# Kernel optimization log

Hardware: AMD Instinct MI355X
Metric: run time of the kernel (lower is better)

The kernel has to match this reference:

```python
import jax, jax.numpy as jnp
import numpy as np

X_DIM, Z_DIM, N_HEIGHT = 256, 256, 32
EPS = 1e-5  # BatchNorm1d eps

def _bn(x, g, b):
    # BatchNorm1d in training mode: batch statistics over the point axis
    m = x.mean(0)
    v = x.var(0)
    return (x - m) * jax.lax.rsqrt(v + EPS) * g + b

def setup_inputs() -> dict:
    key = jax.random.key(0)
    ks = jax.random.split(key, 16)
    B, N, F = 2, 120000, 3
    inp = {
        'pt_fea': jax.random.normal(ks[0], (B, N, F), jnp.float32),
        'grid_ind': jax.random.randint(ks[1], (B, N, 2), 0, 256, dtype=jnp.int32).astype(jnp.int64),
        'occupancy': (jax.random.uniform(ks[2], (B, 1, X_DIM, N_HEIGHT, Z_DIM)) < 0.1).astype(jnp.float32),
    }
    dims = [(3, 64), (64, 128), (128, 256), (256, 512)]
    for i, (di, do) in enumerate(dims):
        inp[f'W{i+1}'] = jax.random.normal(ks[3 + i], (di, do), jnp.float32) * 0.02
        inp[f'b{i+1}'] = jnp.zeros((do,), jnp.float32)
    for i, d in enumerate([3, 64, 128, 256]):
        inp[f'g{i}'] = jnp.ones((d,), jnp.float32)
        inp[f'be{i}'] = jnp.zeros((d,), jnp.float32)
    inp['Wc'] = jax.random.normal(ks[10], (512, 32), jnp.float32) * 0.02
    inp['bc'] = jnp.zeros((32,), jnp.float32)
    return inp

def reference(pt_fea, occupancy, W1, b1, W2, b2, W3, b3, W4, b4,
              g0, be0, g1, be1, g2, be2, g3, be3, Wc, bc, grid_ind):
    B, N, F = pt_fea.shape
    feats = pt_fea.reshape(B * N, F)                          # cat over batch
    # PointNet per-point MLP: BN -> (Linear -> BN -> ReLU) x3 -> Linear
    h = _bn(feats, g0, be0)
    h = jax.nn.relu(_bn(h @ W1 + b1, g1, be1))
    h = jax.nn.relu(_bn(h @ W2 + b2, g2, be2))
    h = jax.nn.relu(_bn(h @ W3 + b3, g3, be3))
    h = h @ W4 + b4                                           # [B*N, 512]

    # linear segment id per (batch, x, z) cell; equivalent to unique+scatter_max
    gi = grid_ind.reshape(B * N, 2).astype(jnp.int32)
    batch_idx = jnp.repeat(jnp.arange(B, dtype=jnp.int32), N)
    seg = batch_idx * (X_DIM * Z_DIM) + gi[:, 0] * Z_DIM + gi[:, 1]
    n_cells = B * X_DIM * Z_DIM

    pooled = jax.ops.segment_max(h, seg, num_segments=n_cells)          # [cells, 512]
    cnt = jax.ops.segment_sum(jnp.ones((B * N,), h.dtype), seg, num_segments=n_cells)
    occ_mask = (cnt > 0)[:, None]
    pooled = jnp.where(occ_mask, pooled, 0.0)                           # kill -inf empties

    # feature compression on occupied cells only; empty cells stay exactly 0
    comp = jax.nn.relu(pooled @ Wc + bc)
    comp = jnp.where(occ_mask, comp, 0.0)                               # [cells, 32]

    bev = comp.reshape(B, X_DIM, Z_DIM, -1).transpose(0, 3, 1, 2)       # [B, 32, X, Z]
    # MaxPool2d(k=3, stride=1, pad=1); -inf padding matches torch's implicit -inf pad
    bev = jax.lax.reduce_window(bev, -jnp.inf, jax.lax.max,
                                (1, 1, 3, 3), (1, 1, 1, 1), 'SAME')

    occu = occupancy[:, 0].transpose(0, 2, 1, 3)                        # [B, H, X, Z]
    out = jnp.concatenate([occu, bev], axis=1)                          # [B, H+32, X, Z]
    return out
```

## Files before the change

kernel.cpp:

```cpp
#include <hip/hip_runtime.h>
#include <hip/hip_bf16.h>

#define EPSN 1e-5f

typedef __bf16 bf16x8 __attribute__((ext_vector_type(8)));
typedef float f32x4 __attribute__((ext_vector_type(4)));

__device__ __forceinline__ unsigned encf(float f) {
  unsigned u = __float_as_uint(f);
  return (u & 0x80000000u) ? ~u : (u | 0x80000000u);
}
__device__ __forceinline__ float decf(unsigned u) {
  return (u & 0x80000000u) ? __uint_as_float(u ^ 0x80000000u) : __uint_as_float(~u);
}

__global__ __launch_bounds__(256) void stats_feats(const float* __restrict__ pt, int n,
                                                   float* __restrict__ sums) {
  float a0 = 0, a1 = 0, a2 = 0, q0 = 0, q1 = 0, q2 = 0;
  for (int p = blockIdx.x * 256 + threadIdx.x; p < n; p += gridDim.x * 256) {
    float v0 = pt[3 * p], v1 = pt[3 * p + 1], v2 = pt[3 * p + 2];
    a0 += v0; a1 += v1; a2 += v2;
    q0 += v0 * v0; q1 += v1 * v1; q2 += v2 * v2;
  }
  __shared__ float red[4][6];
  float vals[6] = {a0, a1, a2, q0, q1, q2};
  int lane = threadIdx.x & 63, wv = threadIdx.x >> 6;
#pragma unroll
  for (int k = 0; k < 6; k++) {
    float v = vals[k];
#pragma unroll
    for (int o = 32; o; o >>= 1) v += __shfl_down(v, o, 64);
    if (lane == 0) red[wv][k] = v;
  }
  __syncthreads();
  if (threadIdx.x < 6) {
    float v = red[0][threadIdx.x] + red[1][threadIdx.x] + red[2][threadIdx.x] + red[3][threadIdx.x];
    atomicAdd(&sums[threadIdx.x], v);
  }
}

__global__ void bn_prep(const float* __restrict__ sums, int C, float invN,
                        const float* __restrict__ g, const float* __restrict__ be,
                        float* __restrict__ sc, float* __restrict__ sh) {
  int c = threadIdx.x;
  if (c < C) {
    float m = sums[c] * invN;
    float v = fmaxf(sums[C + c] * invN - m * m, 0.f);
    float s = g[c] * rsqrtf(v + EPSN);
    sc[c] = s;
    sh[c] = be[c] - m * s;
  }
}

__global__ __launch_bounds__(256) void wconv(const float* __restrict__ W,
                                             __hip_bfloat16* __restrict__ Wt, int K, int C) {
  int idx = blockIdx.x * 256 + threadIdx.x;
  if (idx >= K * C) return;
  int k = idx / C, c = idx - k * C;
  Wt[(size_t)c * K + k] = __float2bfloat16(W[idx]);
}

__global__ __launch_bounds__(256) void gemm1_stats(const float* __restrict__ pt,
                                                   const float* __restrict__ W,
                                                   const float* __restrict__ bias,
                                                   const float* __restrict__ scsh,
                                                   __hip_bfloat16* __restrict__ Y,
                                                   int n, float* __restrict__ sums) {
  const int c = threadIdx.x & 63;
  const float w0 = W[c], w1 = W[64 + c], w2 = W[128 + c], bb = bias[c];
  const float s0 = scsh[0], s1 = scsh[1], s2 = scsh[2];
  const float h0 = scsh[4], h1 = scsh[5], h2 = scsh[6];
  float s = 0.f, q = 0.f;
  const int total = n * 64;
  for (int idx = blockIdx.x * 256 + threadIdx.x; idx < total; idx += gridDim.x * 256) {
    int p = idx >> 6;
    float x0 = s0 * pt[3 * p]     + h0;
    float x1 = s1 * pt[3 * p + 1] + h1;
    float x2 = s2 * pt[3 * p + 2] + h2;
    float y = bb + x0 * w0 + x1 * w1 + x2 * w2;
    Y[idx] = __float2bfloat16(y);
    s += y; q += y * y;
  }
  __shared__ float sred[4][64], qred[4][64];
  int wv = threadIdx.x >> 6;
  sred[wv][c] = s; qred[wv][c] = q;
  __syncthreads();
  if (threadIdx.x < 64) {
    float S = sred[0][c] + sred[1][c] + sred[2][c] + sred[3][c];
    float Q = qred[0][c] + qred[1][c] + qred[2][c] + qred[3][c];
    atomicAdd(&sums[c], S);
    atomicAdd(&sums[64 + c], Q);
  }
}

template <int K>
__global__ __launch_bounds__(256) void gemm_mfma(
    const __hip_bfloat16* __restrict__ Yin, const __hip_bfloat16* __restrict__ Wt,
    const float* __restrict__ bias, const float* __restrict__ sc, const float* __restrict__ sh,
    __hip_bfloat16* __restrict__ Yout, int C, float* __restrict__ sums, int nrows) {
  constexpr int KS = 64, LDA = 72, LDO = 80;
  __shared__ __align__(16) __hip_bfloat16 hA[128 * LDO];
  __shared__ float sredArr[128], qredArr[128];
  const int t = threadIdx.x;
  const int lane = t & 63, wv = t >> 6;
  const int mh = (wv >> 1) * 64, nh = (wv & 1) * 64;
  const int lm = lane & 15, lq = lane >> 4;
  const int p0 = blockIdx.x * 128;
  const int cb0 = blockIdx.y * 128;

  f32x4 acc[4][4];
#pragma unroll
  for (int i = 0; i < 4; i++)
#pragma unroll
    for (int j = 0; j < 4; j++) acc[i][j] = {0.f, 0.f, 0.f, 0.f};

  for (int k0 = 0; k0 < K; k0 += KS) {
    __syncthreads();
#pragma unroll
    for (int it = 0; it < 4; it++) {
      int idx = it * 256 + t;
      int row = idx >> 3;
      int c8 = (idx & 7) * 8;
      int gp = p0 + row;
      __hip_bfloat16 h8[8];
      if (gp < nrows) {
        uint4 raw = *(const uint4*)(Yin + (size_t)gp * K + k0 + c8);
        const __hip_bfloat16* pr = (const __hip_bfloat16*)&raw;
#pragma unroll
        for (int j = 0; j < 8; j++) {
          float v = sc[k0 + c8 + j] * __bfloat162float(pr[j]) + sh[k0 + c8 + j];
          h8[j] = __float2bfloat16(fmaxf(v, 0.f));
        }
      } else {
#pragma unroll
        for (int j = 0; j < 8; j++) h8[j] = __float2bfloat16(0.f);
      }
      *(uint4*)&hA[row * LDA + c8] = *(const uint4*)h8;
    }
    __syncthreads();
#pragma unroll
    for (int kk = 0; kk < KS; kk += 32) {
      bf16x8 a[4], b[4];
#pragma unroll
      for (int i = 0; i < 4; i++)
        a[i] = *(const bf16x8*)&hA[(mh + i * 16 + lm) * LDA + kk + lq * 8];
#pragma unroll
      for (int j = 0; j < 4; j++)
        b[j] = *(const bf16x8*)(const void*)(Wt + (size_t)(cb0 + nh + j * 16 + lm) * K + k0 + kk + lq * 8);
#pragma unroll
      for (int i = 0; i < 4; i++)
#pragma unroll
        for (int j = 0; j < 4; j++)
          acc[i][j] = __builtin_amdgcn_mfma_f32_16x16x32_bf16(a[i], b[j], acc[i][j], 0, 0, 0);
    }
  }

#pragma unroll
  for (int j = 0; j < 4; j++) {
    float bb = bias[cb0 + nh + j * 16 + lm];
#pragma unroll
    for (int i = 0; i < 4; i++)
#pragma unroll
      for (int r = 0; r < 4; r++) acc[i][j][r] += bb;
  }

  __syncthreads();
  if (t < 128) { sredArr[t] = 0.f; qredArr[t] = 0.f; }
  __syncthreads();

#pragma unroll
  for (int j = 0; j < 4; j++) {
    float s = 0.f, q = 0.f;
#pragma unroll
    for (int i = 0; i < 4; i++)
#pragma unroll
      for (int r = 0; r < 4; r++) {
        int grow = p0 + mh + i * 16 + lq * 4 + r;
        if (grow < nrows) { float v = acc[i][j][r]; s += v; q += v * v; }
      }
    s += __shfl_xor(s, 16); s += __shfl_xor(s, 32);
    q += __shfl_xor(q, 16); q += __shfl_xor(q, 32);
    if (lq == 0) {
      atomicAdd(&sredArr[nh + j * 16 + lm], s);
      atomicAdd(&qredArr[nh + j * 16 + lm], q);
    }
  }

  for (int half = 0; half < 2; half++) {
    __syncthreads();
    if ((wv & 1) == half) {
#pragma unroll
      for (int j = 0; j < 4; j++)
#pragma unroll
        for (int i = 0; i < 4; i++)
#pragma unroll
          for (int r = 0; r < 4; r++)
            hA[(mh + i * 16 + lq * 4 + r) * LDO + j * 16 + lm] = __float2bfloat16(acc[i][j][r]);
    }
    __syncthreads();
    int row = t >> 1, seg = t & 1;
    if (p0 + row < nrows) {
      const uint4* src = (const uint4*)&hA[row * LDO + seg * 32];
      uint4* dst = (uint4*)(Yout + (size_t)(p0 + row) * C + cb0 + half * 64 + seg * 32);
      dst[0] = src[0]; dst[1] = src[1]; dst[2] = src[2]; dst[3] = src[3];
    }
  }

  if (t < 128) {
    atomicAdd(&sums[cb0 + t], sredArr[t]);
    atomicAdd(&sums[C + cb0 + t], qredArr[t]);
  }
}

__global__ __launch_bounds__(256) void hist_kernel(const int* __restrict__ gi, int perB,
                                                   unsigned* __restrict__ hist) {
  int b = blockIdx.y;
  int p = blockIdx.x * 256 + threadIdx.x;
  if (p < perB) {
    int gp = b * perB + p;
    int c = (gi[2 * gp] & 255) * 256 + (gi[2 * gp + 1] & 255);
    atomicAdd(&hist[b * 65536 + c], 1u);
  }
}
__global__ __launch_bounds__(256) void scan1(const unsigned* __restrict__ hist,
                                             unsigned* __restrict__ cursor,
                                             unsigned* __restrict__ bSums) {
  __shared__ unsigned s[256];
  int b = blockIdx.y;
  int t = threadIdx.x, i = b * 65536 + blockIdx.x * 256 + t;
  unsigned v = hist[i]; s[t] = v; __syncthreads();
  for (int off = 1; off < 256; off <<= 1) {
    unsigned x = (t >= off) ? s[t - off] : 0u; __syncthreads();
    s[t] += x; __syncthreads();
  }
  cursor[i] = s[t] - v;
  if (t == 255) bSums[b * 256 + blockIdx.x] = s[255];
}
__global__ void scan2(unsigned* __restrict__ bSums) {
  __shared__ unsigned s[256];
  int t = threadIdx.x, i = blockIdx.x * 256 + t;
  unsigned v = bSums[i]; s[t] = v; __syncthreads();
  for (int off = 1; off < 256; off <<= 1) {
    unsigned x = (t >= off) ? s[t - off] : 0u; __syncthreads();
    s[t] += x; __syncthreads();
  }
  bSums[i] = s[t] - v;
}
__global__ __launch_bounds__(256) void mk_starts(const unsigned* __restrict__ cursor,
                                                 const unsigned* __restrict__ bSums,
                                                 unsigned* __restrict__ starts, int perB) {
  int b = blockIdx.y;
  int i = blockIdx.x * 256 + threadIdx.x;
  starts[b * 65537 + i] = cursor[b * 65536 + i] + bSums[b * 256 + (i >> 8)];
  if (i == 0) starts[b * 65537 + 65536] = (unsigned)perB;
}
__global__ __launch_bounds__(256) void scatter_kernel(const int* __restrict__ gi, int perB,
                                                      unsigned* __restrict__ cursor,
                                                      const unsigned* __restrict__ bSums,
                                                      unsigned* __restrict__ sorted,
                                                      unsigned* __restrict__ cells) {
  int b = blockIdx.y;
  int p = blockIdx.x * 256 + threadIdx.x;
  if (p < perB) {
    int gp = b * perB + p;
    int c = (gi[2 * gp] & 255) * 256 + (gi[2 * gp + 1] & 255);
    unsigned pos = atomicAdd(&cursor[b * 65536 + c], 1u) + bSums[b * 256 + (c >> 8)];
    if (pos < (unsigned)perB) {
      sorted[b * perB + pos] = (unsigned)p;
      cells[b * perB + pos] = (unsigned)c;
    }
  }
}

__global__ __launch_bounds__(256, 2) void pool_compress(
    const __hip_bfloat16* __restrict__ Y3, const __hip_bfloat16* __restrict__ Wt4,
    const float* __restrict__ b4, const float* __restrict__ sc, const float* __restrict__ sh,
    const __hip_bfloat16* __restrict__ WcT, const float* __restrict__ bc,
    const unsigned* __restrict__ sortedIdx, const unsigned* __restrict__ sortedCell,
    const unsigned* __restrict__ startsAll, float* __restrict__ comp, int perB) {
  constexpr int K = 256, KS = 64, LDA = 72, MLW = 516;
  __shared__ __align__(16) __hip_bfloat16 hA[64 * LDA];
  __shared__ __align__(16) unsigned maxLds[32 * MLW];
  __shared__ unsigned char slotRow[256];
  __shared__ int rowIdxLds[256];
  const int t = threadIdx.x;
  const int lane = t & 63, wv = t >> 6;
  const int lm = lane & 15, lq = lane >> 4;
  const int batch = blockIdx.y;
  const unsigned* starts = startsAll + batch * 65537;
  const int c0 = blockIdx.x * 32;
  const int r0 = (int)starts[c0];
  int n = (int)starts[c0 + 32] - r0;
  if (n > 256) n = 256;
  if (n < 0) n = 0;
  const int nrg = (n + 63) >> 6;

  for (int i = t; i < n; i += 256) {
    rowIdxLds[i] = (int)sortedIdx[batch * perB + r0 + i] + batch * perB;
    slotRow[i] = (unsigned char)((sortedCell[batch * perB + r0 + i] - c0) & 31);
  }
  for (int i = t; i < 32 * MLW; i += 256) maxLds[i] = 0u;

  for (int rg = 0; rg < nrg; rg++) {
    const int rbase = rg * 64;
    f32x4 acc[4][8];
#pragma unroll
    for (int i = 0; i < 4; i++)
#pragma unroll
      for (int j = 0; j < 8; j++) acc[i][j] = {0.f, 0.f, 0.f, 0.f};
    for (int k0 = 0; k0 < K; k0 += KS) {
      __syncthreads();
#pragma unroll
      for (int it = 0; it < 2; it++) {
        int idx = it * 256 + t;
        int row = idx >> 3;
        int c8 = (idx & 7) * 8;
        int gr = rbase + row;
        __hip_bfloat16 h8[8];
        if (gr < n) {
          uint4 raw = *(const uint4*)(Y3 + (size_t)rowIdxLds[gr] * K + k0 + c8);
          const __hip_bfloat16* pr = (const __hip_bfloat16*)&raw;
#pragma unroll
          for (int j = 0; j < 8; j++) {
            float v = sc[k0 + c8 + j] * __bfloat162float(pr[j]) + sh[k0 + c8 + j];
            h8[j] = __float2bfloat16(fmaxf(v, 0.f));
          }
        } else {
#pragma unroll
          for (int j = 0; j < 8; j++) h8[j] = __float2bfloat16(0.f);
        }
        *(uint4*)&hA[row * LDA + c8] = *(const uint4*)h8;
      }
      __syncthreads();
#pragma unroll
      for (int kk = 0; kk < KS; kk += 32) {
        bf16x8 a[4];
#pragma unroll
        for (int i = 0; i < 4; i++)
          a[i] = *(const bf16x8*)&hA[(i * 16 + lm) * LDA + kk + lq * 8];
#pragma unroll
        for (int j = 0; j < 8; j++) {
          bf16x8 b = *(const bf16x8*)(const void*)(Wt4 + (size_t)(wv * 128 + j * 16 + lm) * K + k0 + kk + lq * 8);
#pragma unroll
          for (int i = 0; i < 4; i++)
            acc[i][j] = __builtin_amdgcn_mfma_f32_16x16x32_bf16(a[i], b, acc[i][j], 0, 0, 0);
        }
      }
    }
#pragma unroll
    for (int j = 0; j < 8; j++) {
      int col = wv * 128 + j * 16 + lm;
#pragma unroll
      for (int i = 0; i < 4; i++) {
#pragma unroll
        for (int r = 0; r < 4; r++) {
          int lrow = rbase + i * 16 + lq * 4 + r;
          if (lrow < n)
            atomicMax(&maxLds[(int)slotRow[lrow] * MLW + col], encf(acc[i][j][r]));
        }
      }
    }
  }
  __syncthreads();

  if (wv < 2) {
    f32x4 accC[2];
    accC[0] = {0.f, 0.f, 0.f, 0.f};
    accC[1] = {0.f, 0.f, 0.f, 0.f};
#pragma unroll
    for (int ks = 0; ks < 16; ks++) {
      int koff = ks * 32 + lq * 8;
      const unsigned* mp = &maxLds[(wv * 16 + lm) * MLW + koff];
      uint4 m0 = *(const uint4*)mp;
      uint4 m1 = *(const uint4*)(mp + 4);
      unsigned mu[8] = {m0.x, m0.y, m0.z, m0.w, m1.x, m1.y, m1.z, m1.w};
      __hip_bfloat16 af[8];
#pragma unroll
      for (int j = 0; j < 8; j++)
        af[j] = __float2bfloat16(decf(mu[j]) + b4[koff + j]);
      bf16x8 aa = *(const bf16x8*)af;
#pragma unroll
      for (int jn = 0; jn < 2; jn++) {
        bf16x8 b = *(const bf16x8*)(const void*)(WcT + (size_t)(jn * 16 + lm) * 512 + koff);
        accC[jn] = __builtin_amdgcn_mfma_f32_16x16x32_bf16(aa, b, accC[jn], 0, 0, 0);
      }
    }
#pragma unroll
    for (int jn = 0; jn < 2; jn++) {
      float bb = bc[jn * 16 + lm];
#pragma unroll
      for (int r = 0; r < 4; r++) {
        int cell = c0 + wv * 16 + lq * 4 + r;
        int occ = starts[cell + 1] > starts[cell];
        float v = occ ? fmaxf(accC[jn][r] + bb, 0.f) : 0.f;
        comp[((size_t)batch * 65536 + cell) * 32 + jn * 16 + lm] = v;
      }
    }
  }
}

__global__ __launch_bounds__(256) void maxpool_write(const float* __restrict__ comp,
                                                     float* __restrict__ out) {
  __shared__ float tile[32][65];
  int bid = blockIdx.x;
  int z0 = (bid & 3) * 64, x = (bid >> 2) & 255, b = bid >> 10;
  int f = threadIdx.x & 31, zs = threadIdx.x >> 5;
  for (int zi = 0; zi < 8; zi++) {
    int z = z0 + zi * 8 + zs;
    float m = -3.402823466e38f;
    for (int dx = -1; dx <= 1; dx++) {
      int xx = x + dx;
      if (xx < 0 || xx > 255) continue;
      for (int dz = -1; dz <= 1; dz++) {
        int zz = z + dz;
        if (zz < 0 || zz > 255) continue;
        m = fmaxf(m, comp[(size_t)((b << 16) + (xx << 8) + zz) * 32 + f]);
      }
    }
    tile[f][zi * 8 + zs] = m;
  }
  __syncthreads();
  int f2 = threadIdx.x >> 3, seg = threadIdx.x & 7;
  float* dst = out + ((size_t)(b * 64 + 32 + f2) * 256 + x) * 256 + z0 + seg * 8;
#pragma unroll
  for (int u = 0; u < 8; u++) dst[u] = tile[f2][seg * 8 + u];
}

__global__ __launch_bounds__(256) void occu_write(const float* __restrict__ occ,
                                                  float* __restrict__ out) {
  int idx = blockIdx.x * 256 + threadIdx.x;
  int z = idx & 255, x = (idx >> 8) & 255, hh = (idx >> 16) & 31, b = idx >> 21;
  out[((size_t)(b * 64 + hh) * 256 + x) * 256 + z] =
      occ[((size_t)((b * 256 + x) * 32 + hh)) * 256 + z];
}

extern "C" void kernel_launch(void* const* d_in, const int* in_sizes, int n_in,
                              void* d_out, int out_size, void* d_ws, size_t ws_size,
                              hipStream_t stream) {
  const float* pt_fea   = (const float*)d_in[0];
  const int*   grid_ind = (const int*)d_in[1];
  const float* occup    = (const float*)d_in[2];
  const float* W1 = (const float*)d_in[3];  const float* b1 = (const float*)d_in[4];
  const float* W2 = (const float*)d_in[5];  const float* b2 = (const float*)d_in[6];
  const float* W3 = (const float*)d_in[7];  const float* b3 = (const float*)d_in[8];
  const float* W4 = (const float*)d_in[9];  const float* b4 = (const float*)d_in[10];
  const float* g0 = (const float*)d_in[11]; const float* be0 = (const float*)d_in[12];
  const float* g1 = (const float*)d_in[13]; const float* be1 = (const float*)d_in[14];
  const float* g2 = (const float*)d_in[15]; const float* be2 = (const float*)d_in[16];
  const float* g3 = (const float*)d_in[17]; const float* be3 = (const float*)d_in[18];
  const float* Wc = (const float*)d_in[19]; const float* bc = (const float*)d_in[20];
  float* out = (float*)d_out;

  const int nPts = in_sizes[0] / 3;
  const int perB = nPts / 2;
  const float invN = 1.f / (float)nPts;

  char* ws = (char*)d_ws;
  float* stats = (float*)ws;
  float* scsh  = (float*)(ws + 4096);
  float* sums0 = stats;        float* sums1 = stats + 16;
  float* sums2 = stats + 160;  float* sums3 = stats + 416;
  float* sc0 = scsh;
  float* sc1 = scsh + 16;   float* sh1 = scsh + 80;
  float* sc2 = scsh + 144;  float* sh2 = scsh + 272;
  float* sc3 = scsh + 400;  float* sh3 = scsh + 656;
  __hip_bfloat16* Wt2 = (__hip_bfloat16*)(ws + 8192);
  __hip_bfloat16* Wt3 = (__hip_bfloat16*)(ws + 24576);
  __hip_bfloat16* Wt4 = (__hip_bfloat16*)(ws + 90112);
  __hip_bfloat16* WcT = (__hip_bfloat16*)(ws + 352256);
  char* S0 = ws + 385024;
  __hip_bfloat16* Y1 = (__hip_bfloat16*)S0;
  __hip_bfloat16* Y2 = (__hip_bfloat16*)(S0 + 30720000ll);
  __hip_bfloat16* Y3 = (__hip_bfloat16*)(S0 + 92160000ll);
  float* comp       = (float*)S0;
  char* sortBase    = S0 + 16777216ll;
  unsigned* hist    = (unsigned*)sortBase;
  unsigned* cursor  = hist + 2 * 65536;
  unsigned* bSums   = cursor + 2 * 65536;
  unsigned* startsA = bSums + 1024;
  unsigned* sorted  = startsA + 131080;
  unsigned* cells   = sorted + 2 * perB;

  hipMemsetAsync(stats, 0, 4096, stream);

  wconv<<<(64 * 128 + 255) / 256, 256, 0, stream>>>(W2, Wt2, 64, 128);
  wconv<<<(128 * 256 + 255) / 256, 256, 0, stream>>>(W3, Wt3, 128, 256);
  wconv<<<(256 * 512 + 255) / 256, 256, 0, stream>>>(W4, Wt4, 256, 512);
  wconv<<<(512 * 32 + 255) / 256, 256, 0, stream>>>(Wc, WcT, 512, 32);

  stats_feats<<<256, 256, 0, stream>>>(pt_fea, nPts, sums0);
  bn_prep<<<1, 256, 0, stream>>>(sums0, 3, invN, g0, be0, sc0, scsh + 4);

  gemm1_stats<<<512, 256, 0, stream>>>(pt_fea, W1, b1, scsh, Y1, nPts, sums1);
  bn_prep<<<1, 256, 0, stream>>>(sums1, 64, invN, g1, be1, sc1, sh1);

  gemm_mfma<64><<<dim3(nPts / 128, 1), 256, 0, stream>>>(Y1, Wt2, b2, sc1, sh1, Y2, 128, sums2, nPts);
  bn_prep<<<1, 256, 0, stream>>>(sums2, 128, invN, g2, be2, sc2, sh2);

  gemm_mfma<128><<<dim3(nPts / 128, 2), 256, 0, stream>>>(Y2, Wt3, b3, sc2, sh2, Y3, 256, sums3, nPts);
  bn_prep<<<1, 256, 0, stream>>>(sums3, 256, invN, g3, be3, sc3, sh3);

  hipMemsetAsync(hist, 0, 2 * 65536 * 4, stream);
  const int pgrid = (perB + 255) / 256;
  hist_kernel<<<dim3(pgrid, 2), 256, 0, stream>>>(grid_ind, perB, hist);
  scan1<<<dim3(256, 2), 256, 0, stream>>>(hist, cursor, bSums);
  scan2<<<2, 256, 0, stream>>>(bSums);
  mk_starts<<<dim3(256, 2), 256, 0, stream>>>(cursor, bSums, startsA, perB);
  scatter_kernel<<<dim3(pgrid, 2), 256, 0, stream>>>(grid_ind, perB, cursor, bSums, sorted, cells);

  pool_compress<<<dim3(2048, 2), 256, 0, stream>>>(
      Y3, Wt4, b4, sc3, sh3, WcT, bc, sorted, cells, startsA, comp, perB);

  maxpool_write<<<2048, 256, 0, stream>>>(comp, out);
  occu_write<<<16384, 256, 0, stream>>>(occup, out);
}
```

Before: 728.8 us.

## Shrink pool_compress tiles to 16 cells and preload gathered rows into registers

The pooling/compression kernel now handles 16 cells per block instead of 32, with 32-row groups and a smaller row cap. This roughly halves its shared memory, which should allow more resident blocks per CU, and the grid doubles to match. Each thread now fetches its whole 256-wide gathered feature row into registers once per row group rather than reloading a slice every k-step. LDS zeroing is vectorised and the final 512→32 compression is split so each wave computes one 16-column half. The trade-off is less reuse of the W4 fragments per block, plus a lower cap on rows per block that could truncate very dense cells.

```diff
diff --git a/kernel.cpp b/kernel.cpp
--- a/kernel.cpp
+++ b/kernel.cpp
@@ -272,77 +272,87 @@
   }
 }
 
-__global__ __launch_bounds__(256, 2) void pool_compress(
+__global__ __launch_bounds__(256) void pool_compress(
     const __hip_bfloat16* __restrict__ Y3, const __hip_bfloat16* __restrict__ Wt4,
     const float* __restrict__ b4, const float* __restrict__ sc, const float* __restrict__ sh,
     const __hip_bfloat16* __restrict__ WcT, const float* __restrict__ bc,
     const unsigned* __restrict__ sortedIdx, const unsigned* __restrict__ sortedCell,
     const unsigned* __restrict__ startsAll, float* __restrict__ comp, int perB) {
-  constexpr int K = 256, KS = 64, LDA = 72, MLW = 516;
-  __shared__ __align__(16) __hip_bfloat16 hA[64 * LDA];
-  __shared__ __align__(16) unsigned maxLds[32 * MLW];
-  __shared__ unsigned char slotRow[256];
-  __shared__ int rowIdxLds[256];
+  constexpr int K = 256, LDA = 72, MLW = 516, MAXN = 192;
+  __shared__ __align__(16) __hip_bfloat16 hA[32 * LDA];
+  __shared__ __align__(16) unsigned maxLds[16 * MLW];
+  __shared__ unsigned char slotRow[MAXN];
+  __shared__ int rowIdxLds[MAXN];
   const int t = threadIdx.x;
   const int lane = t & 63, wv = t >> 6;
   const int lm = lane & 15, lq = lane >> 4;
   const int batch = blockIdx.y;
   const unsigned* starts = startsAll + batch * 65537;
-  const int c0 = blockIdx.x * 32;
+  const int c0 = blockIdx.x * 16;
   const int r0 = (int)starts[c0];
-  int n = (int)starts[c0 + 32] - r0;
-  if (n > 256) n = 256;
+  int n = (int)starts[c0 + 16] - r0;
+  if (n > MAXN) n = MAXN;
   if (n < 0) n = 0;
-  const int nrg = (n + 63) >> 6;
+  const int nrg = (n + 31) >> 5;
 
   for (int i = t; i < n; i += 256) {
     rowIdxLds[i] = (int)sortedIdx[batch * perB + r0 + i] + batch * perB;
-    slotRow[i] = (unsigned char)((sortedCell[batch * perB + r0 + i] - c0) & 31);
-  }
-  for (int i = t; i < 32 * MLW; i += 256) maxLds[i] = 0u;
+    slotRow[i] = (unsigned char)((sortedCell[batch * perB + r0 + i] - c0) & 15);
+  }
+  {
+    const uint4 z4 = {0u, 0u, 0u, 0u};
+    for (int i = t * 4; i < 16 * MLW; i += 1024) *(uint4*)&maxLds[i] = z4;
+  }
+  __syncthreads();
+
+  const int srow = t >> 3;
+  const int c8 = (t & 7) * 8;
 
   for (int rg = 0; rg < nrg; rg++) {
-    const int rbase = rg * 64;
-    f32x4 acc[4][8];
-#pragma unroll
-    for (int i = 0; i < 4; i++)
+    const int rbase = rg * 32;
+    const int gr = rbase + srow;
+    uint4 g[4];
+    if (gr < n) {
+      const __hip_bfloat16* src = Y3 + (size_t)rowIdxLds[gr] * K + c8;
+#pragma unroll
+      for (int q = 0; q < 4; q++) g[q] = *(const uint4*)(src + q * 64);
+    } else {
+#pragma unroll
+      for (int q = 0; q < 4; q++) g[q] = {0u, 0u, 0u, 0u};
+    }
+
+    f32x4 acc[2][8];
+#pragma unroll
+    for (int i = 0; i < 2; i++)
 #pragma unroll
       for (int j = 0; j < 8; j++) acc[i][j] = {0.f, 0.f, 0.f, 0.f};
-    for (int k0 = 0; k0 < K; k0 += KS) {
+
+#pragma unroll
+    for (int k0q = 0; k0q < 4; k0q++) {
       __syncthreads();
-#pragma unroll
-      for (int it = 0; it < 2; it++) {
-        int idx = it * 256 + t;
-        int row = idx >> 3;
-        int c8 = (idx & 7) * 8;
-        int gr = rbase + row;
+      {
+        const __hip_bfloat16* pr = (const __hip_bfloat16*)&g[k0q];
+        const int colb = k0q * 64 + c8;
         __hip_bfloat16 h8[8];
-        if (gr < n) {
-          uint4 raw = *(const uint4*)(Y3 + (size_t)rowIdxLds[gr] * K + k0 + c8);
-          const __hip_bfloat16* pr = (const __hip_bfloat16*)&raw;
-#pragma unroll
-          for (int j = 0; j < 8; j++) {
-            float v = sc[k0 + c8 + j] * __bfloat162float(pr[j]) + sh[k0 + c8 + j];
-            h8[j] = __float2bfloat16(fmaxf(v, 0.f));
-          }
-        } else {
-#pragma unroll
-          for (int j = 0; j < 8; j++) h8[j] = __float2bfloat16(0.f);
+#pragma unroll
+        for (int e = 0; e < 8; e++) {
+          float v = fmaf(sc[colb + e], __bfloat162float(pr[e]), sh[colb + e]);
+          h8[e] = __float2bfloat16(fmaxf(v, 0.f));
         }
-        *(uint4*)&hA[row * LDA + c8] = *(const uint4*)h8;
+        *(uint4*)&hA[srow * LDA + c8] = *(const uint4*)h8;
       }
       __syncthreads();
 #pragma unroll
-      for (int kk = 0; kk < KS; kk += 32) {
-        bf16x8 a[4];
-#pragma unroll
-        for (int i = 0; i < 4; i++)
+      for (int kk = 0; kk < 64; kk += 32) {
+        bf16x8 a[2];
+#pragma unroll
+        for (int i = 0; i < 2; i++)
           a[i] = *(const bf16x8*)&hA[(i * 16 + lm) * LDA + kk + lq * 8];
 #pragma unroll
         for (int j = 0; j < 8; j++) {
-          bf16x8 b = *(const bf16x8*)(const void*)(Wt4 + (size_t)(wv * 128 + j * 16 + lm) * K + k0 + kk + lq * 8);
-#pragma unroll
-          for (int i = 0; i < 4; i++)
+          bf16x8 b = *(const bf16x8*)(const void*)(Wt4 + (size_t)(wv * 128 + j * 16 + lm) * K + k0q * 64 + kk + lq * 8);
+#pragma unroll
+          for (int i = 0; i < 2; i++)
             acc[i][j] = __builtin_amdgcn_mfma_f32_16x16x32_bf16(a[i], b, acc[i][j], 0, 0, 0);
         }
       }
@@ -351,7 +361,7 @@
     for (int j = 0; j < 8; j++) {
       int col = wv * 128 + j * 16 + lm;
 #pragma unroll
-      for (int i = 0; i < 4; i++) {
+      for (int i = 0; i < 2; i++) {
 #pragma unroll
         for (int r = 0; r < 4; r++) {
           int lrow = rbase + i * 16 + lq * 4 + r;
@@ -364,13 +374,11 @@
   __syncthreads();
 
   if (wv < 2) {
-    f32x4 accC[2];
-    accC[0] = {0.f, 0.f, 0.f, 0.f};
-    accC[1] = {0.f, 0.f, 0.f, 0.f};
+    f32x4 accC = {0.f, 0.f, 0.f, 0.f};
 #pragma unroll
     for (int ks = 0; ks < 16; ks++) {
       int koff = ks * 32 + lq * 8;
-      const unsigned* mp = &maxLds[(wv * 16 + lm) * MLW + koff];
+      const unsigned* mp = &maxLds[lm * MLW + koff];
       uint4 m0 = *(const uint4*)mp;
       uint4 m1 = *(const uint4*)(mp + 4);
       unsigned mu[8] = {m0.x, m0.y, m0.z, m0.w, m1.x, m1.y, m1.z, m1.w};
@@ -379,22 +387,16 @@
       for (int j = 0; j < 8; j++)
         af[j] = __float2bfloat16(decf(mu[j]) + b4[koff + j]);
       bf16x8 aa = *(const bf16x8*)af;
-#pragma unroll
-      for (int jn = 0; jn < 2; jn++) {
-        bf16x8 b = *(const bf16x8*)(const void*)(WcT + (size_t)(jn * 16 + lm) * 512 + koff);
-        accC[jn] = __builtin_amdgcn_mfma_f32_16x16x32_bf16(aa, b, accC[jn], 0, 0, 0);
-      }
-    }
-#pragma unroll
-    for (int jn = 0; jn < 2; jn++) {
-      float bb = bc[jn * 16 + lm];
-#pragma unroll
-      for (int r = 0; r < 4; r++) {
-        int cell = c0 + wv * 16 + lq * 4 + r;
-        int occ = starts[cell + 1] > starts[cell];
-        float v = occ ? fmaxf(accC[jn][r] + bb, 0.f) : 0.f;
-        comp[((size_t)batch * 65536 + cell) * 32 + jn * 16 + lm] = v;
-      }
+      bf16x8 b = *(const bf16x8*)(const void*)(WcT + (size_t)(wv * 16 + lm) * 512 + koff);
+      accC = __builtin_amdgcn_mfma_f32_16x16x32_bf16(aa, b, accC, 0, 0, 0);
+    }
+    float bb = bc[wv * 16 + lm];
+#pragma unroll
+    for (int r = 0; r < 4; r++) {
+      int cell = c0 + lq * 4 + r;
+      int occ = starts[cell + 1] > starts[cell];
+      float v = occ ? fmaxf(accC[r] + bb, 0.f) : 0.f;
+      comp[((size_t)batch * 65536 + cell) * 32 + wv * 16 + lm] = v;
     }
   }
 }
@@ -508,7 +510,7 @@
   mk_starts<<<dim3(256, 2), 256, 0, stream>>>(cursor, bSums, startsA, perB);
   scatter_kernel<<<dim3(pgrid, 2), 256, 0, stream>>>(grid_ind, perB, cursor, bSums, sorted, cells);
 
-  pool_compress<<<dim3(2048, 2), 256, 0, stream>>>(
+  pool_compress<<<dim3(4096, 2), 256, 0, stream>>>(
       Y3, Wt4, b4, sc3, sh3, WcT, bc, sorted, cells, startsA, comp, perB);
 
   maxpool_write<<<2048, 256, 0, stream>>>(comp, out);
```

Result: slower. 1.003 ms (+37.6%).

## Write layer-3 activations in cell-sorted order so pooling reads contiguously

Applied to the files above, without the earlier changes.

Moves the counting sort ahead of the third GEMM and has the scatter produce an inverse permutation. The GEMM epilogue writes each output row straight to its sorted position, so pool_compress reads Y3 rows contiguously instead of gathering through an index list. This trades scattered 512-byte row writes in the GEMM for contiguous, coalesced reads in the pooling kernel, and drops the sorted-index buffer. Overflowing positions are clamped to the last slot, which could overwrite a row if counts ever exceed perB.

```diff
diff --git a/kernel.cpp b/kernel.cpp
--- a/kernel.cpp
+++ b/kernel.cpp
@@ -97,7 +97,8 @@
 __global__ __launch_bounds__(256) void gemm_mfma(
     const __hip_bfloat16* __restrict__ Yin, const __hip_bfloat16* __restrict__ Wt,
     const float* __restrict__ bias, const float* __restrict__ sc, const float* __restrict__ sh,
-    __hip_bfloat16* __restrict__ Yout, int C, float* __restrict__ sums, int nrows) {
+    __hip_bfloat16* __restrict__ Yout, int C, float* __restrict__ sums, int nrows,
+    const unsigned* __restrict__ perm) {
   constexpr int KS = 64, LDA = 72, LDO = 80;
   __shared__ __align__(16) __hip_bfloat16 hA[128 * LDO];
   __shared__ float sredArr[128], qredArr[128];
@@ -199,9 +200,11 @@
     }
     __syncthreads();
     int row = t >> 1, seg = t & 1;
-    if (p0 + row < nrows) {
+    int gp = p0 + row;
+    if (gp < nrows) {
+      size_t drow = perm ? (size_t)perm[gp] : (size_t)gp;
       const uint4* src = (const uint4*)&hA[row * LDO + seg * 32];
-      uint4* dst = (uint4*)(Yout + (size_t)(p0 + row) * C + cb0 + half * 64 + seg * 32);
+      uint4* dst = (uint4*)(Yout + drow * C + cb0 + half * 64 + seg * 32);
       dst[0] = src[0]; dst[1] = src[1]; dst[2] = src[2]; dst[3] = src[3];
     }
   }
@@ -257,18 +260,17 @@
 __global__ __launch_bounds__(256) void scatter_kernel(const int* __restrict__ gi, int perB,
                                                       unsigned* __restrict__ cursor,
                                                       const unsigned* __restrict__ bSums,
-                                                      unsigned* __restrict__ sorted,
-                                                      unsigned* __restrict__ cells) {
+                                                      unsigned* __restrict__ cells,
+                                                      unsigned* __restrict__ invPos) {
   int b = blockIdx.y;
   int p = blockIdx.x * 256 + threadIdx.x;
   if (p < perB) {
     int gp = b * perB + p;
     int c = (gi[2 * gp] & 255) * 256 + (gi[2 * gp + 1] & 255);
     unsigned pos = atomicAdd(&cursor[b * 65536 + c], 1u) + bSums[b * 256 + (c >> 8)];
-    if (pos < (unsigned)perB) {
-      sorted[b * perB + pos] = (unsigned)p;
-      cells[b * perB + pos] = (unsigned)c;
-    }
+    if (pos >= (unsigned)perB) pos = (unsigned)perB - 1u;
+    cells[b * perB + pos] = (unsigned)c;
+    invPos[gp] = (unsigned)(b * perB) + pos;
   }
 }
 
@@ -276,13 +278,12 @@
     const __hip_bfloat16* __restrict__ Y3, const __hip_bfloat16* __restrict__ Wt4,
     const float* __restrict__ b4, const float* __restrict__ sc, const float* __restrict__ sh,
     const __hip_bfloat16* __restrict__ WcT, const float* __restrict__ bc,
-    const unsigned* __restrict__ sortedIdx, const unsigned* __restrict__ sortedCell,
-    const unsigned* __restrict__ startsAll, float* __restrict__ comp, int perB) {
+    const unsigned* __restrict__ sortedCell, const unsigned* __restrict__ startsAll,
+    float* __restrict__ comp, int perB) {
   constexpr int K = 256, KS = 64, LDA = 72, MLW = 516;
   __shared__ __align__(16) __hip_bfloat16 hA[64 * LDA];
   __shared__ __align__(16) unsigned maxLds[32 * MLW];
   __shared__ unsigned char slotRow[256];
-  __shared__ int rowIdxLds[256];
   const int t = threadIdx.x;
   const int lane = t & 63, wv = t >> 6;
   const int lm = lane & 15, lq = lane >> 4;
@@ -294,11 +295,10 @@
   if (n > 256) n = 256;
   if (n < 0) n = 0;
   const int nrg = (n + 63) >> 6;
-
-  for (int i = t; i < n; i += 256) {
-    rowIdxLds[i] = (int)sortedIdx[batch * perB + r0 + i] + batch * perB;
+  const size_t rowBase = (size_t)batch * perB + r0;
+
+  for (int i = t; i < n; i += 256)
     slotRow[i] = (unsigned char)((sortedCell[batch * perB + r0 + i] - c0) & 31);
-  }
   for (int i = t; i < 32 * MLW; i += 256) maxLds[i] = 0u;
 
   for (int rg = 0; rg < nrg; rg++) {
@@ -318,7 +318,7 @@
         int gr = rbase + row;
         __hip_bfloat16 h8[8];
         if (gr < n) {
-          uint4 raw = *(const uint4*)(Y3 + (size_t)rowIdxLds[gr] * K + k0 + c8);
+          uint4 raw = *(const uint4*)(Y3 + (rowBase + gr) * K + k0 + c8);
           const __hip_bfloat16* pr = (const __hip_bfloat16*)&raw;
 #pragma unroll
           for (int j = 0; j < 8; j++) {
@@ -473,13 +473,13 @@
   __hip_bfloat16* Y2 = (__hip_bfloat16*)(S0 + 30720000ll);
   __hip_bfloat16* Y3 = (__hip_bfloat16*)(S0 + 92160000ll);
   float* comp       = (float*)S0;
-  char* sortBase    = S0 + 16777216ll;
+  char* sortBase    = S0 + 17000000ll;
   unsigned* hist    = (unsigned*)sortBase;
   unsigned* cursor  = hist + 2 * 65536;
   unsigned* bSums   = cursor + 2 * 65536;
   unsigned* startsA = bSums + 1024;
-  unsigned* sorted  = startsA + 131080;
-  unsigned* cells   = sorted + 2 * perB;
+  unsigned* cells   = startsA + 131080;
+  unsigned* invPos  = cells + 2 * perB;
 
   hipMemsetAsync(stats, 0, 4096, stream);
 
@@ -494,11 +494,8 @@
   gemm1_stats<<<512, 256, 0, stream>>>(pt_fea, W1, b1, scsh, Y1, nPts, sums1);
   bn_prep<<<1, 256, 0, stream>>>(sums1, 64, invN, g1, be1, sc1, sh1);
 
-  gemm_mfma<64><<<dim3(nPts / 128, 1), 256, 0, stream>>>(Y1, Wt2, b2, sc1, sh1, Y2, 128, sums2, nPts);
+  gemm_mfma<64><<<dim3(nPts / 128, 1), 256, 0, stream>>>(Y1, Wt2, b2, sc1, sh1, Y2, 128, sums2, nPts, nullptr);
   bn_prep<<<1, 256, 0, stream>>>(sums2, 128, invN, g2, be2, sc2, sh2);
-
-  gemm_mfma<128><<<dim3(nPts / 128, 2), 256, 0, stream>>>(Y2, Wt3, b3, sc2, sh2, Y3, 256, sums3, nPts);
-  bn_prep<<<1, 256, 0, stream>>>(sums3, 256, invN, g3, be3, sc3, sh3);
 
   hipMemsetAsync(hist, 0, 2 * 65536 * 4, stream);
   const int pgrid = (perB + 255) / 256;
@@ -506,10 +503,13 @@
   scan1<<<dim3(256, 2), 256, 0, stream>>>(hist, cursor, bSums);
   scan2<<<2, 256, 0, stream>>>(bSums);
   mk_starts<<<dim3(256, 2), 256, 0, stream>>>(cursor, bSums, startsA, perB);
-  scatter_kernel<<<dim3(pgrid, 2), 256, 0, stream>>>(grid_ind, perB, cursor, bSums, sorted, cells);
+  scatter_kernel<<<dim3(pgrid, 2), 256, 0, stream>>>(grid_ind, perB, cursor, bSums, cells, invPos);
+
+  gemm_mfma<128><<<dim3(nPts / 128, 2), 256, 0, stream>>>(Y2, Wt3, b3, sc2, sh2, Y3, 256, sums3, nPts, invPos);
+  bn_prep<<<1, 256, 0, stream>>>(sums3, 256, invN, g3, be3, sc3, sh3);
 
   pool_compress<<<dim3(2048, 2), 256, 0, stream>>>(
-      Y3, Wt4, b4, sc3, sh3, WcT, bc, sorted, cells, startsA, comp, perB);
+      Y3, Wt4, b4, sc3, sh3, WcT, bc, cells, startsA, comp, perB);
 
   maxpool_write<<<2048, 256, 0, stream>>>(comp, out);
   occu_write<<<16384, 256, 0, stream>>>(occup, out);
```

After: 723.9 us. No clear change (-0.7%).
